# Optimization experiments

Hardware: AMD Instinct MI355X
Metric: run time of the kernel (lower is better)

## Reference

```python
import jax, jax.numpy as jnp
import numpy as np

P = 100   # num_proxies
N = 1024  # num_samples
D = 512


def _edge_index():
    # complete bipartite proxy<->sample graph, both directions, plus self-loops
    # (PyG GATConv adds self-loops for all nodes by default)
    p = np.arange(P)
    s = np.arange(P, P + N)
    src_ps = np.repeat(p, N)   # proxy -> sample
    dst_ps = np.tile(s, P)
    loops = np.arange(P + N)
    src = np.concatenate([src_ps, dst_ps, loops]).astype(np.int32)
    dst = np.concatenate([dst_ps, src_ps, loops]).astype(np.int32)
    return jnp.asarray(src), jnp.asarray(dst)


def setup_inputs() -> dict:
    key = jax.random.key(0)
    ks = jax.random.split(key, 10)
    sc = 1.0 / np.sqrt(D)
    src, dst = _edge_index()
    return {
        "x": jax.random.normal(ks[0], (N, D), jnp.float32),
        "proxies": jax.random.normal(ks[1], (P, D), jnp.float32),
        "W1": jax.random.normal(ks[2], (D, D), jnp.float32) * sc,
        "a_src1": jax.random.normal(ks[3], (D,), jnp.float32) * sc,
        "a_dst1": jax.random.normal(ks[4], (D,), jnp.float32) * sc,
        "b1": jnp.zeros((D,), jnp.float32),
        "W2": jax.random.normal(ks[5], (D, D), jnp.float32) * sc,
        "a_src2": jax.random.normal(ks[6], (D,), jnp.float32) * sc,
        "a_dst2": jax.random.normal(ks[7], (D,), jnp.float32) * sc,
        "b2": jnp.zeros((D,), jnp.float32),
        "fc_w": jax.random.normal(ks[8], (D, 100), jnp.float32) * sc,
        "fc_b": jnp.zeros((100,), jnp.float32),
        "src": src,
        "dst": dst,
    }


def _gat_conv(x, src, dst, W, a_src, a_dst, b, n_nodes):
    # PyG GATConv, heads=1, concat=True, negative_slope=0.2
    h = x @ W                      # [n, D]
    l_src = h @ a_src              # [n]
    l_dst = h @ a_dst              # [n]
    e = jax.nn.leaky_relu(l_src[src] + l_dst[dst], 0.2)   # [E]
    # segment softmax over edges sharing the same destination
    e = e - jax.ops.segment_max(e, dst, num_segments=n_nodes)[dst]
    ex = jnp.exp(e)
    denom = jax.ops.segment_sum(ex, dst, num_segments=n_nodes)[dst]
    alpha = ex / denom             # [E]
    out = jax.ops.segment_sum(alpha[:, None] * h[src], dst, num_segments=n_nodes)
    return out + b


def reference(x, proxies, W1, a_src1, a_dst1, b1, W2, a_src2, a_dst2, b2, fc_w, fc_b, src, dst):
    n = P + N
    h = jnp.concatenate([proxies, x], axis=0)          # [P+N, D]
    h = jax.nn.relu(_gat_conv(h, src, dst, W1, a_src1, a_dst1, b1, n))
    # Dropout -> identity (eval)
    h = jax.nn.relu(_gat_conv(h, src, dst, W2, a_src2, a_dst2, b2, n))
    preds = h @ fc_w + fc_b                            # [P+N, 100]
    return preds[P:], h[P:]
```

## Files before the change

kernel.cpp:

```cpp
#include <hip/hip_runtime.h>

#define PP 100
#define NS 1024
#define NN 1124
#define DD 512
#define CC 100
#define NTHR 256

typedef _Float16 f16;
typedef _Float16 f16x8 __attribute__((ext_vector_type(8)));
typedef float    f32x4 __attribute__((ext_vector_type(4)));

__device__ __forceinline__ float lk(float v) { return v > 0.f ? v : 0.2f * v; }
__device__ __forceinline__ f16 hif(float v) { return (f16)v; }
__device__ __forceinline__ f16 lof(float v) { return (f16)(v - (float)((f16)v)); }


__device__ __forceinline__ void mgemm_core(
    const f16* __restrict__ Ah, const f16* __restrict__ Al,
    const f16* __restrict__ Bth, const f16* __restrict__ Btl,
    int K, int row0, int col0, f16* __restrict__ lds, f32x4 acc[2][2])
{
  const int t = threadIdx.x;
  const int lane = t & 63, w = t >> 6;
  const int wr = w >> 1, wc = w & 1;
  const int srow = t >> 2, su = t & 3;
  const size_t aoff = (size_t)(row0 + srow) * K + su * 8;
  const size_t boff = (size_t)(col0 + srow) * K + su * 8;
  const int lw = srow * 40 + su * 8;
  const int fra = wr * 32 + (lane & 15);
  const int frb = wc * 32 + (lane & 15);
  const int fu  = (lane >> 4) * 8;
  f32x4 pa0 = *(const f32x4*)(Ah + aoff);
  f32x4 pa1 = *(const f32x4*)(Al + aoff);
  f32x4 pb0 = *(const f32x4*)(Bth + boff);
  f32x4 pb1 = *(const f32x4*)(Btl + boff);
  *(f32x4*)(lds + 0    + lw) = pa0;
  *(f32x4*)(lds + 2560 + lw) = pa1;
  *(f32x4*)(lds + 5120 + lw) = pb0;
  *(f32x4*)(lds + 7680 + lw) = pb1;
  if (K > 32) {
    pa0 = *(const f32x4*)(Ah + aoff + 32);
    pa1 = *(const f32x4*)(Al + aoff + 32);
    pb0 = *(const f32x4*)(Bth + boff + 32);
    pb1 = *(const f32x4*)(Btl + boff + 32);
  }
  __syncthreads();
  int cur = 0;
  for (int kt = 32; kt <= K; kt += 32) {
    f16* rb = lds + cur * 10240;
    f16* wb = lds + (cur ^ 1) * 10240;
    f16x8 ah[2], al[2], bh[2], bl[2];
#pragma unroll
    for (int m = 0; m < 2; ++m) {
      ah[m] = *(const f16x8*)(rb + (fra + m * 16) * 40 + fu);
      al[m] = *(const f16x8*)(rb + 2560 + (fra + m * 16) * 40 + fu);
    }
#pragma unroll
    for (int n = 0; n < 2; ++n) {
      bh[n] = *(const f16x8*)(rb + 5120 + (frb + n * 16) * 40 + fu);
      bl[n] = *(const f16x8*)(rb + 7680 + (frb + n * 16) * 40 + fu);
    }
    if (kt < K) {
      *(f32x4*)(wb + 0    + lw) = pa0;
      *(f32x4*)(wb + 2560 + lw) = pa1;
      *(f32x4*)(wb + 5120 + lw) = pb0;
      *(f32x4*)(wb + 7680 + lw) = pb1;
      if (kt + 32 < K) {
        pa0 = *(const f32x4*)(Ah + aoff + kt + 32);
        pa1 = *(const f32x4*)(Al + aoff + kt + 32);
        pb0 = *(const f32x4*)(Bth + boff + kt + 32);
        pb1 = *(const f32x4*)(Btl + boff + kt + 32);
      }
    }
#pragma unroll
    for (int m = 0; m < 2; ++m)
#pragma unroll
      for (int n = 0; n < 2; ++n) {
        acc[m][n] = __builtin_amdgcn_mfma_f32_16x16x32_f16(ah[m], bh[n], acc[m][n], 0, 0, 0);
        acc[m][n] = __builtin_amdgcn_mfma_f32_16x16x32_f16(al[m], bh[n], acc[m][n], 0, 0, 0);
        acc[m][n] = __builtin_amdgcn_mfma_f32_16x16x32_f16(ah[m], bl[n], acc[m][n], 0, 0, 0);
      }
    __syncthreads();
    cur ^= 1;
  }
}

__device__ __forceinline__ void agg_core(
    const float* __restrict__ lsrc, int kvalid,
    const float* __restrict__ ldb, const float* __restrict__ lsb,
    const f16* __restrict__ Bth, const f16* __restrict__ Btl,
    int K, int row0, int col0, int rvalid,
    const float* __restrict__ selfv,
    f16* __restrict__ outh, f16* __restrict__ outl,
    f16* __restrict__ lds, float* __restrict__ fred)
{
  const int t = threadIdx.x, lane = t & 63, w = t >> 6;
  const int wr = w >> 1, wc = w & 1;
  float* zred = fred;
  float* res  = fred + 256;
  float* riz  = fred + 320;
  const int srow = t >> 2, su = t & 3;
  float sm = -1e30f;
  for (int k = t; k < kvalid; k += NTHR) sm = fmaxf(sm, lsrc[k]);
#pragma unroll
  for (int off = 1; off < 64; off <<= 1) sm = fmaxf(sm, __shfl_xor(sm, off));
  if (lane == 0) zred[w] = sm;
  __syncthreads();
  sm = fmaxf(fmaxf(zred[0], zred[1]), fmaxf(zred[2], zred[3]));
  __syncthreads();
  const bool rok = (row0 + srow) < rvalid;
  float ldr = 0.f, mr = 0.f;
  if (rok) {
    ldr = ldb[row0 + srow];
    mr  = lk(fmaxf(sm, lsb[row0 + srow]) + ldr);
  }
  const size_t boff = (size_t)(col0 + srow) * K + su * 8;
  const int lw = srow * 40 + su * 8;
  const int fra = wr * 32 + (lane & 15);
  const int frb = wc * 32 + (lane & 15);
  const int fu  = (lane >> 4) * 8;
  f32x4 acc[2][2] = {};
  float zacc = 0.f;
  f32x4 pl0 = *(const f32x4*)(lsrc + su * 8);
  f32x4 pl1 = *(const f32x4*)(lsrc + su * 8 + 4);
  f32x4 pb0 = *(const f32x4*)(Bth + boff);
  f32x4 pb1 = *(const f32x4*)(Btl + boff);
  {
    f16x8 ae, al8;
#pragma unroll
    for (int j = 0; j < 8; ++j) {
      const int k = su * 8 + j;
      const float lv = (j < 4) ? pl0[j] : pl1[j - 4];
      float f = 0.f;
      if (rok && k < kvalid) f = __expf(lk(lv + ldr) - mr);
      zacc += f;
      ae[j] = hif(f); al8[j] = lof(f);
    }
    *(f16x8*)(lds + 0    + lw) = ae;
    *(f16x8*)(lds + 2560 + lw) = al8;
    *(f32x4*)(lds + 5120 + lw) = pb0;
    *(f32x4*)(lds + 7680 + lw) = pb1;
  }
  if (K > 32) {
    pl0 = *(const f32x4*)(lsrc + 32 + su * 8);
    pl1 = *(const f32x4*)(lsrc + 32 + su * 8 + 4);
    pb0 = *(const f32x4*)(Bth + boff + 32);
    pb1 = *(const f32x4*)(Btl + boff + 32);
  }
  __syncthreads();
  int cur = 0;
  for (int kt = 32; kt <= K; kt += 32) {
    f16* rb = lds + cur * 10240;
    f16* wb = lds + (cur ^ 1) * 10240;
    f16x8 ah[2], alr[2], bh[2], bl[2];
#pragma unroll
    for (int m = 0; m < 2; ++m) {
      ah[m]  = *(const f16x8*)(rb + (fra + m * 16) * 40 + fu);
      alr[m] = *(const f16x8*)(rb + 2560 + (fra + m * 16) * 40 + fu);
    }
#pragma unroll
    for (int n = 0; n < 2; ++n) {
      bh[n] = *(const f16x8*)(rb + 5120 + (frb + n * 16) * 40 + fu);
      bl[n] = *(const f16x8*)(rb + 7680 + (frb + n * 16) * 40 + fu);
    }
    if (kt < K) {
      f16x8 ae, al8;
      const int k0 = kt + su * 8;
#pragma unroll
      for (int j = 0; j < 8; ++j) {
        const int k = k0 + j;
        const float lv = (j < 4) ? pl0[j] : pl1[j - 4];
        float f = 0.f;
        if (rok && k < kvalid) f = __expf(lk(lv + ldr) - mr);
        zacc += f;
        ae[j] = hif(f); al8[j] = lof(f);
      }
      *(f16x8*)(wb + 0    + lw) = ae;
      *(f16x8*)(wb + 2560 + lw) = al8;
      *(f32x4*)(wb + 5120 + lw) = pb0;
      *(f32x4*)(wb + 7680 + lw) = pb1;
      if (kt + 32 < K) {
        pl0 = *(const f32x4*)(lsrc + kt + 32 + su * 8);
        pl1 = *(const f32x4*)(lsrc + kt + 32 + su * 8 + 4);
        pb0 = *(const f32x4*)(Bth + boff + kt + 32);
        pb1 = *(const f32x4*)(Btl + boff + kt + 32);
      }
    }
#pragma unroll
    for (int m = 0; m < 2; ++m)
#pragma unroll
      for (int n = 0; n < 2; ++n) {
        acc[m][n] = __builtin_amdgcn_mfma_f32_16x16x32_f16(ah[m],  bh[n], acc[m][n], 0, 0, 0);
        acc[m][n] = __builtin_amdgcn_mfma_f32_16x16x32_f16(alr[m], bh[n], acc[m][n], 0, 0, 0);
        acc[m][n] = __builtin_amdgcn_mfma_f32_16x16x32_f16(ah[m],  bl[n], acc[m][n], 0, 0, 0);
      }
    __syncthreads();
    cur ^= 1;
  }
  zred[t] = zacc;
  __syncthreads();
  if (t < 64) {
    float z = zred[t * 4] + zred[t * 4 + 1] + zred[t * 4 + 2] + zred[t * 4 + 3];
    float es = 0.f, iz = 0.f;
    if (row0 + t < rvalid) {
      const float l2 = ldb[row0 + t], s2 = lsb[row0 + t];
      const float m2 = lk(fmaxf(sm, s2) + l2);
      es = __expf(lk(s2 + l2) - m2);
      iz = 1.f / (z + es);
    }
    res[t] = es; riz[t] = iz;
  }
  __syncthreads();
#pragma unroll
  for (int m = 0; m < 2; ++m)
#pragma unroll
    for (int q = 0; q < 4; ++q) {
      const int rl = wr * 32 + m * 16 + (lane >> 4) * 4 + q;
      const int gr = row0 + rl;
      if (gr >= rvalid) continue;
      const float es = res[rl], iz = riz[rl];
#pragma unroll
      for (int n = 0; n < 2; ++n) {
        const int c = col0 + wc * 32 + n * 16 + (lane & 15);
        const float v = (acc[m][n][q] + es * selfv[(size_t)gr * DD + c]) * iz;
        outh[(size_t)gr * DD + c] = hif(v);
        outl[(size_t)gr * DD + c] = lof(v);
      }
    }
}

__device__ __forceinline__ void cvt_tile(
    const float* __restrict__ in, int R, int Cin,
    f16* __restrict__ oh, f16* __restrict__ ol, int ldo,
    int ti, int tj)
{
  const int t = threadIdx.x;
  const int gj0 = tj * 64 + (t & 31) * 2;
  const int i8  = (t >> 5) * 8;
  const bool c0 = gj0 < Cin, c1 = (gj0 + 1) < Cin;
  f16x8 vh0, vl0, vh1, vl1;
#pragma unroll
  for (int e = 0; e < 8; ++e) {
    const int gi = ti * 64 + i8 + e;
    float a = 0.f, b = 0.f;
    if (gi < R) {
      if (c0 && c1) {
        const float2 v = *(const float2*)(in + (size_t)gi * Cin + gj0);
        a = v.x; b = v.y;
      } else if (c0) {
        a = in[(size_t)gi * Cin + gj0];
      }
    }
    vh0[e] = hif(a); vl0[e] = lof(a);
    vh1[e] = hif(b); vl1[e] = lof(b);
  }
  const size_t o0 = (size_t)gj0 * ldo + ti * 64 + i8;
  *(f16x8*)(oh + o0) = vh0;
  *(f16x8*)(ol + o0) = vl0;
  const size_t o1 = o0 + ldo;
  *(f16x8*)(oh + o1) = vh1;
  *(f16x8*)(ol + o1) = vl1;
}

__global__ __launch_bounds__(NTHR) void prep1_k(
    const float* __restrict__ W1, const float* __restrict__ W2,
    const float* __restrict__ as1, const float* __restrict__ ad1,
    const float* __restrict__ as2, const float* __restrict__ ad2,
    float* __restrict__ v1s, float* __restrict__ v1d,
    float* __restrict__ v2s, float* __restrict__ v2d,
    float* __restrict__ ls2, float* __restrict__ ld2)
{
  const int u = blockIdx.x;
  if (u < 256) {
    const int wid  = u * 4 + (threadIdx.x >> 6);
    const int lane = threadIdx.x & 63;
    const int r = wid & 511;
    const bool l1 = (wid < 512);
    const float* W = l1 ? W1 : W2;
    const float4* a4 = (const float4*)(l1 ? as1 : as2);
    const float4* b4 = (const float4*)(l1 ? ad1 : ad2);
    const float4* w4 = (const float4*)(W + (size_t)r * DD);
    float4 w0 = w4[lane], w1 = w4[lane + 64];
    float4 a0 = a4[lane], a1 = a4[lane + 64];
    float4 b0 = b4[lane], b1 = b4[lane + 64];
    float s1 = w0.x * a0.x + w0.y * a0.y + w0.z * a0.z + w0.w * a0.w
             + w1.x * a1.x + w1.y * a1.y + w1.z * a1.z + w1.w * a1.w;
    float s2 = w0.x * b0.x + w0.y * b0.y + w0.z * b0.z + w0.w * b0.w
             + w1.x * b1.x + w1.y * b1.y + w1.z * b1.z + w1.w * b1.w;
#pragma unroll
    for (int off = 32; off > 0; off >>= 1) {
      s1 += __shfl_down(s1, off);
      s2 += __shfl_down(s2, off);
    }
    if (lane == 0) {
      (l1 ? v1s : v2s)[r] = s1;
      (l1 ? v1d : v2d)[r] = s2;
    }
  } else {
    for (int i = threadIdx.x; i < 1152; i += NTHR) { ls2[i] = 0.f; ld2[i] = 0.f; }
  }
}

__global__ __launch_bounds__(NTHR) void prep2_k(
    const float* __restrict__ x, const float* __restrict__ prox,
    const float* __restrict__ W1, const float* __restrict__ W2,
    const float* __restrict__ fcw,
    const float* __restrict__ v1s, const float* __restrict__ v1d,
    f16* xth, f16* xtl, f16* pth, f16* ptl,
    f16* W1th, f16* W1tl, f16* W2th, f16* W2tl, f16* fwth, f16* fwtl,
    float* __restrict__ ls1, float* __restrict__ ld1)
{
  const int b = blockIdx.x;
  if (b < 64) {
    cvt_tile(W1, 512, 512, W1th, W1tl, 512, b >> 3, b & 7);
  } else if (b < 128) {
    cvt_tile(W2, 512, 512, W2th, W2tl, 512, (b - 64) >> 3, (b - 64) & 7);
  } else if (b < 256) {
    cvt_tile(x, NS, 512, xth, xtl, NS, (b - 128) >> 3, (b - 128) & 7);
  } else if (b < 272) {
    cvt_tile(prox, PP, 512, pth, ptl, 128, (b - 256) >> 3, (b - 256) & 7);
  } else if (b < 288) {
    cvt_tile(fcw, 512, CC, fwth, fwtl, 512, (b - 272) >> 1, (b - 272) & 1);
  } else {
    const int r    = (b - 288) * 4 + (threadIdx.x >> 6);
    const int lane = threadIdx.x & 63;
    if (r >= NN) return;
    const float* row = (r < PP) ? prox + (size_t)r * DD
                                : x + (size_t)(r - PP) * DD;
    const float4* r4 = (const float4*)row;
    const float4* s4 = (const float4*)v1s;
    const float4* d4 = (const float4*)v1d;
    float4 v0 = r4[lane], v1 = r4[lane + 64];
    float4 a0 = s4[lane], a1 = s4[lane + 64];
    float4 b0 = d4[lane], b1 = d4[lane + 64];
    float s1 = v0.x * a0.x + v0.y * a0.y + v0.z * a0.z + v0.w * a0.w
             + v1.x * a1.x + v1.y * a1.y + v1.z * a1.z + v1.w * a1.w;
    float s2 = v0.x * b0.x + v0.y * b0.y + v0.z * b0.z + v0.w * b0.w
             + v1.x * b1.x + v1.y * b1.y + v1.z * b1.z + v1.w * b1.w;
#pragma unroll
    for (int off = 32; off > 0; off >>= 1) {
      s1 += __shfl_down(s1, off);
      s2 += __shfl_down(s2, off);
    }
    if (lane == 0) { ls1[r] = s1; ld1[r] = s2; }
  }
}

__global__ __launch_bounds__(NTHR) void agg1x_k(
    const float* __restrict__ ls1, const float* __restrict__ ld1,
    const f16* __restrict__ pth, const f16* __restrict__ ptl,
    const f16* __restrict__ xth, const f16* __restrict__ xtl,
    const float* __restrict__ x, const float* __restrict__ prox,
    f16* __restrict__ M1h, f16* __restrict__ M1l)
{
  __shared__ __align__(16) f16 lds[20480];
  __shared__ float fred[384];
  const int b = blockIdx.x;
  if (b < 128) {
    const int row0 = (b >> 3) * 64, col0 = (b & 7) * 64;
    agg_core(ls1, PP, ld1 + PP, ls1 + PP, pth, ptl, 128, row0, col0, NS,
             x, M1h + (size_t)PP * DD, M1l + (size_t)PP * DD, lds, fred);
  } else {
    const int b2 = b - 128;
    const int row0 = (b2 >> 3) * 64, col0 = (b2 & 7) * 64;
    agg_core(ls1 + PP, NS, ld1, ls1, xth, xtl, NS, row0, col0, PP,
             prox, M1h, M1l, lds, fred);
  }
}

__global__ __launch_bounds__(NTHR) void h1_k(
    const f16* __restrict__ M1h, const f16* __restrict__ M1l,
    const f16* __restrict__ W1th, const f16* __restrict__ W1tl,
    const float* __restrict__ b1,
    const float* __restrict__ v2s, const float* __restrict__ v2d,
    float* __restrict__ h1, f16* __restrict__ h1pth, f16* __restrict__ h1ptl,
    float* __restrict__ ls2, float* __restrict__ ld2)
{
  __shared__ __align__(16) f16 lds[20480];
  f32x4 acc[2][2] = {};
  const int t = threadIdx.x, lane = t & 63, w = t >> 6, wr = w >> 1, wc = w & 1;
  const int b = blockIdx.x;
  const int row0 = (b >> 3) * 64, col0 = (b & 7) * 64;
  mgemm_core(M1h, M1l, W1th, W1tl, DD, row0, col0, lds, acc);
  const int c0 = col0 + wc * 32 + (lane & 15);
  const int c1 = c0 + 16;
  const float vs0 = v2s[c0], vs1 = v2s[c1];
  const float vd0 = v2d[c0], vd1 = v2d[c1];
  const float bb0 = b1[c0],  bb1 = b1[c1];
#pragma unroll
  for (int m = 0; m < 2; ++m)
#pragma unroll
    for (int q = 0; q < 4; ++q) {
      const int r = row0 + wr * 32 + m * 16 + (lane >> 4) * 4 + q;
      if (r >= NN) continue;
      float ps = 0.f, pd = 0.f;
#pragma unroll
      for (int n = 0; n < 2; ++n) {
        const int c = (n == 0) ? c0 : c1;
        const float v = fmaxf(acc[m][n][q] + (n == 0 ? bb0 : bb1), 0.f);
        h1[(size_t)r * DD + c] = v;
        ps += v * (n == 0 ? vs0 : vs1);
        pd += v * (n == 0 ? vd0 : vd1);
        if (r < 128) {
          const size_t o = (size_t)c * 128 + r;
          f16 hh = (f16)0.f, ll = (f16)0.f;
          if (r < PP) { hh = hif(v); ll = lof(v); }
          h1pth[o] = hh; h1ptl[o] = ll;
        }
      }
#pragma unroll
      for (int off = 1; off < 16; off <<= 1) {
        ps += __shfl_xor(ps, off);
        pd += __shfl_xor(pd, off);
      }
      if ((lane & 15) == 0) {
        atomicAdd(&ls2[r], ps);
        atomicAdd(&ld2[r], pd);
      }
    }
}

__global__ __launch_bounds__(NTHR) void agg2x_k(
    const float* __restrict__ ls2, const float* __restrict__ ld2,
    const f16* __restrict__ h1pth, const f16* __restrict__ h1ptl,
    const float* __restrict__ h1,
    f16* __restrict__ M2h, f16* __restrict__ M2l)
{
  __shared__ __align__(16) f16 lds[20480];
  __shared__ float fred[384];
  const int b = blockIdx.x;
  const int row0 = (b >> 3) * 64, col0 = (b & 7) * 64;
  agg_core(ls2, PP, ld2 + PP, ls2 + PP, h1pth, h1ptl, 128, row0, col0, NS,
           h1 + (size_t)PP * DD, M2h, M2l, lds, fred);
}

__global__ __launch_bounds__(NTHR) void h2_k(
    const f16* __restrict__ M2h, const f16* __restrict__ M2l,
    const f16* __restrict__ W2th, const f16* __restrict__ W2tl,
    const float* __restrict__ b2, float* __restrict__ h2s,
    f16* __restrict__ h2h, f16* __restrict__ h2l)
{
  __shared__ __align__(16) f16 lds[20480];
  f32x4 acc[2][2] = {};
  const int t = threadIdx.x, lane = t & 63, w = t >> 6, wr = w >> 1, wc = w & 1;
  const int b = blockIdx.x;
  const int row0 = (b >> 3) * 64, col0 = (b & 7) * 64;
  mgemm_core(M2h, M2l, W2th, W2tl, DD, row0, col0, lds, acc);
#pragma unroll
  for (int m = 0; m < 2; ++m)
#pragma unroll
    for (int q = 0; q < 4; ++q) {
      const int r = row0 + wr * 32 + m * 16 + (lane >> 4) * 4 + q;
#pragma unroll
      for (int n = 0; n < 2; ++n) {
        const int c = col0 + wc * 32 + n * 16 + (lane & 15);
        const float v = fmaxf(acc[m][n][q] + b2[c], 0.f);
        const size_t o = (size_t)r * DD + c;
        h2s[o] = v;
        h2h[o] = hif(v); h2l[o] = lof(v);
      }
    }
}

__global__ __launch_bounds__(NTHR) void fc_k(
    const f16* __restrict__ h2h, const f16* __restrict__ h2l,
    const f16* __restrict__ fwth, const f16* __restrict__ fwtl,
    const float* __restrict__ fcb, float* __restrict__ out)
{
  __shared__ __align__(16) f16 lds[20480];
  f32x4 acc[2][2] = {};
  const int t = threadIdx.x, lane = t & 63, w = t >> 6, wr = w >> 1, wc = w & 1;
  const int b = blockIdx.x;
  const int row0 = (b >> 1) * 64, col0 = (b & 1) * 64;
  mgemm_core(h2h, h2l, fwth, fwtl, DD, row0, col0, lds, acc);
#pragma unroll
  for (int m = 0; m < 2; ++m)
#pragma unroll
    for (int q = 0; q < 4; ++q) {
      const int r = row0 + wr * 32 + m * 16 + (lane >> 4) * 4 + q;
#pragma unroll
      for (int n = 0; n < 2; ++n) {
        const int c = col0 + wc * 32 + n * 16 + (lane & 15);
        if (c < CC) out[(size_t)r * CC + c] = acc[m][n][q] + fcb[c];
      }
    }
}

extern "C" void kernel_launch(void* const* d_in, const int* in_sizes, int n_in,
                              void* d_out, int out_size, void* d_ws, size_t ws_size,
                              hipStream_t stream)
{
  const float* x    = (const float*)d_in[0];
  const float* prox = (const float*)d_in[1];
  const float* W1   = (const float*)d_in[2];
  const float* as1  = (const float*)d_in[3];
  const float* ad1  = (const float*)d_in[4];
  const float* b1   = (const float*)d_in[5];
  const float* W2   = (const float*)d_in[6];
  const float* as2  = (const float*)d_in[7];
  const float* ad2  = (const float*)d_in[8];
  const float* b2   = (const float*)d_in[9];
  const float* fcw  = (const float*)d_in[10];
  const float* fcb  = (const float*)d_in[11];
  float* out = (float*)d_out;

  float* F = (float*)d_ws;
  float* h1   = F; F += (size_t)NN * DD;
  float* ls1  = F; F += 1152;
  float* ld1  = F; F += 1152;
  float* ls2  = F; F += 1152;
  float* ld2  = F; F += 1152;
  float* v1s  = F; F += DD;
  float* v1d  = F; F += DD;
  float* v2s  = F; F += DD;
  float* v2d  = F; F += DD;
  f16* H = (f16*)F;
  f16* M1h  = H; H += (size_t)1152 * DD;
  f16* M1l  = H; H += (size_t)1152 * DD;
  f16* M2h  = H; H += (size_t)NS * DD;
  f16* M2l  = H; H += (size_t)NS * DD;
  f16* xth  = H; H += (size_t)DD * NS;
  f16* xtl  = H; H += (size_t)DD * NS;
  f16* pth  = H; H += (size_t)DD * 128;
  f16* ptl  = H; H += (size_t)DD * 128;
  f16* W1th = H; H += (size_t)DD * DD;
  f16* W1tl = H; H += (size_t)DD * DD;
  f16* W2th = H; H += (size_t)DD * DD;
  f16* W2tl = H; H += (size_t)DD * DD;
  f16* fwth = H; H += (size_t)128 * DD;
  f16* fwtl = H; H += (size_t)128 * DD;
  f16* h2h  = H; H += (size_t)NS * DD;
  f16* h2l  = H; H += (size_t)NS * DD;
  f16* h1pth = H; H += (size_t)DD * 128;
  f16* h1ptl = H; H += (size_t)DD * 128;
  float* h2s = out + (size_t)NS * CC;

  dim3 blk(NTHR);
  prep1_k<<<dim3(257), blk, 0, stream>>>(W1, W2, as1, ad1, as2, ad2,
                                         v1s, v1d, v2s, v2d, ls2, ld2);
  prep2_k<<<dim3(569), blk, 0, stream>>>(x, prox, W1, W2, fcw, v1s, v1d,
      xth, xtl, pth, ptl, W1th, W1tl, W2th, W2tl, fwth, fwtl, ls1, ld1);
  agg1x_k<<<dim3(144), blk, 0, stream>>>(ls1, ld1, pth, ptl, xth, xtl,
                                         x, prox, M1h, M1l);
  h1_k<<<dim3(144), blk, 0, stream>>>(M1h, M1l, W1th, W1tl, b1, v2s, v2d,
                                      h1, h1pth, h1ptl, ls2, ld2);
  agg2x_k<<<dim3(128), blk, 0, stream>>>(ls2, ld2, h1pth, h1ptl, h1, M2h, M2l);
  h2_k<<<dim3(128), blk, 0, stream>>>(M2h, M2l, W2th, W2tl, b2, h2s, h2h, h2l);
  fc_k<<<dim3(32), blk, 0, stream>>>(h2h, h2l, fwth, fwtl, fcb, out);
}
```

Measured before the change: 151.6 us.

## Split proxy-row aggregation over K chunks with atomics, normalize in h1 GEMM

The proxy-destination aggregation in layer 1 (100 rows summing over 1024 samples) used to be done by 16 blocks each running the full K=1024 loop. It now splits K into four 256-wide chunks across 64 blocks. Each block atomically adds its unnormalized partial sums into an fp32 buffer, along with the softmax denominators. The self-loop term and the 1/Z normalization move into the h1 GEMM's A-tile load, which converts the fp32 partials to split f16 on the fly. The cost is extra zeroing blocks in prep1, fp32 atomics, and more per-tile work in h1_k.

```diff
diff --git a/kernel.cpp b/kernel.cpp
--- a/kernel.cpp
+++ b/kernel.cpp
@@ -269,7 +269,8 @@
     const float* __restrict__ as2, const float* __restrict__ ad2,
     float* __restrict__ v1s, float* __restrict__ v1d,
     float* __restrict__ v2s, float* __restrict__ v2d,
-    float* __restrict__ ls2, float* __restrict__ ld2)
+    float* __restrict__ ls2, float* __restrict__ ld2,
+    float* __restrict__ M1pf, float* __restrict__ zP)
 {
   const int u = blockIdx.x;
   if (u < 256) {
@@ -297,8 +298,16 @@
       (l1 ? v1s : v2s)[r] = s1;
       (l1 ? v1d : v2d)[r] = s2;
     }
+  } else if (u == 256) {
+    for (int i = threadIdx.x; i < 1152; i += NTHR) { ls2[i] = 0.f; ld2[i] = 0.f; }
+    if (threadIdx.x < 128) zP[threadIdx.x] = 0.f;
   } else {
-    for (int i = threadIdx.x; i < 1152; i += NTHR) { ls2[i] = 0.f; ld2[i] = 0.f; }
+    float4* p4 = (float4*)M1pf + (size_t)(u - 257) * 800;
+#pragma unroll
+    for (int p = 0; p < 4; ++p) {
+      const int i = threadIdx.x + p * 256;
+      if (i < 800) p4[i] = make_float4(0.f, 0.f, 0.f, 0.f);
+    }
   }
 }
 
@@ -351,7 +360,8 @@
     const float* __restrict__ ls1, const float* __restrict__ ld1,
     const f16* __restrict__ pth, const f16* __restrict__ ptl,
     const f16* __restrict__ xth, const f16* __restrict__ xtl,
-    const float* __restrict__ x, const float* __restrict__ prox,
+    const float* __restrict__ x,
+    float* __restrict__ M1pf, float* __restrict__ zP,
     f16* __restrict__ M1h, f16* __restrict__ M1l)
 {
   __shared__ __align__(16) f16 lds[20480];
@@ -361,16 +371,138 @@
     const int row0 = (b >> 3) * 64, col0 = (b & 7) * 64;
     agg_core(ls1, PP, ld1 + PP, ls1 + PP, pth, ptl, 128, row0, col0, NS,
              x, M1h + (size_t)PP * DD, M1l + (size_t)PP * DD, lds, fred);
-  } else {
-    const int b2 = b - 128;
-    const int row0 = (b2 >> 3) * 64, col0 = (b2 & 7) * 64;
-    agg_core(ls1 + PP, NS, ld1, ls1, xth, xtl, NS, row0, col0, PP,
-             prox, M1h, M1l, lds, fred);
-  }
+    return;
+  }
+  const int t = threadIdx.x, lane = t & 63, w = t >> 6;
+  const int wr = w >> 1, wc = w & 1;
+  const int b2 = b - 128;
+  const int tile = b2 >> 2, chunk = b2 & 3;
+  const int row0 = (tile >> 3) * 64, col0 = (tile & 7) * 64;
+  const int k0 = chunk * 256;
+  const float* lsrc = ls1 + PP;
+  float sm = -1e30f;
+  for (int k = t; k < NS; k += NTHR) sm = fmaxf(sm, lsrc[k]);
+#pragma unroll
+  for (int off = 1; off < 64; off <<= 1) sm = fmaxf(sm, __shfl_xor(sm, off));
+  if (lane == 0) fred[w] = sm;
+  __syncthreads();
+  sm = fmaxf(fmaxf(fred[0], fred[1]), fmaxf(fred[2], fred[3]));
+  __syncthreads();
+  const int srow = t >> 2, su = t & 3;
+  const bool rok = (row0 + srow) < PP;
+  float ldr = 0.f, mr = 0.f;
+  if (rok) {
+    ldr = ld1[row0 + srow];
+    mr  = lk(fmaxf(sm, ls1[row0 + srow]) + ldr);
+  }
+  const size_t boff = (size_t)(col0 + srow) * NS + k0 + su * 8;
+  const int lw = srow * 40 + su * 8;
+  const int fra = wr * 32 + (lane & 15);
+  const int frb = wc * 32 + (lane & 15);
+  const int fu  = (lane >> 4) * 8;
+  f32x4 acc[2][2] = {};
+  float zacc = 0.f;
+  f32x4 pl0 = *(const f32x4*)(lsrc + k0 + su * 8);
+  f32x4 pl1 = *(const f32x4*)(lsrc + k0 + su * 8 + 4);
+  f32x4 pb0 = *(const f32x4*)(xth + boff);
+  f32x4 pb1 = *(const f32x4*)(xtl + boff);
+  {
+    f16x8 ae, al8;
+#pragma unroll
+    for (int j = 0; j < 8; ++j) {
+      const float lv = (j < 4) ? pl0[j] : pl1[j - 4];
+      float f = 0.f;
+      if (rok) f = __expf(lk(lv + ldr) - mr);
+      zacc += f;
+      ae[j] = hif(f); al8[j] = lof(f);
+    }
+    *(f16x8*)(lds + 0    + lw) = ae;
+    *(f16x8*)(lds + 2560 + lw) = al8;
+    *(f32x4*)(lds + 5120 + lw) = pb0;
+    *(f32x4*)(lds + 7680 + lw) = pb1;
+  }
+  pl0 = *(const f32x4*)(lsrc + k0 + 32 + su * 8);
+  pl1 = *(const f32x4*)(lsrc + k0 + 32 + su * 8 + 4);
+  pb0 = *(const f32x4*)(xth + boff + 32);
+  pb1 = *(const f32x4*)(xtl + boff + 32);
+  __syncthreads();
+  int cur = 0;
+  for (int kt = 32; kt <= 256; kt += 32) {
+    f16* rb = lds + cur * 10240;
+    f16* wb = lds + (cur ^ 1) * 10240;
+    f16x8 ah[2], alr[2], bh[2], bl[2];
+#pragma unroll
+    for (int m = 0; m < 2; ++m) {
+      ah[m]  = *(const f16x8*)(rb + (fra + m * 16) * 40 + fu);
+      alr[m] = *(const f16x8*)(rb + 2560 + (fra + m * 16) * 40 + fu);
+    }
+#pragma unroll
+    for (int n = 0; n < 2; ++n) {
+      bh[n] = *(const f16x8*)(rb + 5120 + (frb + n * 16) * 40 + fu);
+      bl[n] = *(const f16x8*)(rb + 7680 + (frb + n * 16) * 40 + fu);
+    }
+    if (kt < 256) {
+      f16x8 ae, al8;
+#pragma unroll
+      for (int j = 0; j < 8; ++j) {
+        const float lv = (j < 4) ? pl0[j] : pl1[j - 4];
+        float f = 0.f;
+        if (rok) f = __expf(lk(lv + ldr) - mr);
+        zacc += f;
+        ae[j] = hif(f); al8[j] = lof(f);
+      }
+      *(f16x8*)(wb + 0    + lw) = ae;
+      *(f16x8*)(wb + 2560 + lw) = al8;
+      *(f32x4*)(wb + 5120 + lw) = pb0;
+      *(f32x4*)(wb + 7680 + lw) = pb1;
+      if (kt + 32 < 256) {
+        pl0 = *(const f32x4*)(lsrc + k0 + kt + 32 + su * 8);
+        pl1 = *(const f32x4*)(lsrc + k0 + kt + 32 + su * 8 + 4);
+        pb0 = *(const f32x4*)(xth + boff + kt + 32);
+        pb1 = *(const f32x4*)(xtl + boff + kt + 32);
+      }
+    }
+#pragma unroll
+    for (int m = 0; m < 2; ++m)
+#pragma unroll
+      for (int n = 0; n < 2; ++n) {
+        acc[m][n] = __builtin_amdgcn_mfma_f32_16x16x32_f16(ah[m],  bh[n], acc[m][n], 0, 0, 0);
+        acc[m][n] = __builtin_amdgcn_mfma_f32_16x16x32_f16(alr[m], bh[n], acc[m][n], 0, 0, 0);
+        acc[m][n] = __builtin_amdgcn_mfma_f32_16x16x32_f16(ah[m],  bl[n], acc[m][n], 0, 0, 0);
+      }
+    __syncthreads();
+    cur ^= 1;
+  }
+  if (col0 == 0) {
+    fred[t] = zacc;
+    __syncthreads();
+    if (t < 64) {
+      const int r = row0 + t;
+      if (r < PP) {
+        float z = fred[t * 4] + fred[t * 4 + 1] + fred[t * 4 + 2] + fred[t * 4 + 3];
+        atomicAdd(&zP[r], z);
+      }
+    }
+  }
+#pragma unroll
+  for (int m = 0; m < 2; ++m)
+#pragma unroll
+    for (int q = 0; q < 4; ++q) {
+      const int gr = row0 + wr * 32 + m * 16 + (lane >> 4) * 4 + q;
+      if (gr >= PP) continue;
+#pragma unroll
+      for (int n = 0; n < 2; ++n) {
+        const int c = col0 + wc * 32 + n * 16 + (lane & 15);
+        atomicAdd(&M1pf[(size_t)gr * DD + c], acc[m][n][q]);
+      }
+    }
 }
 
 __global__ __launch_bounds__(NTHR) void h1_k(
     const f16* __restrict__ M1h, const f16* __restrict__ M1l,
+    const float* __restrict__ M1pf, const float* __restrict__ zP,
+    const float* __restrict__ ls1, const float* __restrict__ ld1,
+    const float* __restrict__ prox,
     const f16* __restrict__ W1th, const f16* __restrict__ W1tl,
     const float* __restrict__ b1,
     const float* __restrict__ v2s, const float* __restrict__ v2d,
@@ -378,11 +510,121 @@
     float* __restrict__ ls2, float* __restrict__ ld2)
 {
   __shared__ __align__(16) f16 lds[20480];
-  f32x4 acc[2][2] = {};
+  __shared__ float fred[384];
+  float* esA = fred + 256;
+  float* izA = fred + 320;
   const int t = threadIdx.x, lane = t & 63, w = t >> 6, wr = w >> 1, wc = w & 1;
   const int b = blockIdx.x;
   const int row0 = (b >> 3) * 64, col0 = (b & 7) * 64;
-  mgemm_core(M1h, M1l, W1th, W1tl, DD, row0, col0, lds, acc);
+  const bool hasP = (row0 < 128);
+  if (hasP) {
+    float sm = -1e30f;
+    for (int k = t; k < NS; k += NTHR) sm = fmaxf(sm, ls1[PP + k]);
+#pragma unroll
+    for (int off = 1; off < 64; off <<= 1) sm = fmaxf(sm, __shfl_xor(sm, off));
+    if (lane == 0) fred[w] = sm;
+    __syncthreads();
+    sm = fmaxf(fmaxf(fred[0], fred[1]), fmaxf(fred[2], fred[3]));
+    if (t < 64) {
+      const int r = row0 + t;
+      float es = 0.f, iz = 0.f;
+      if (r < PP) {
+        const float ldr = ld1[r];
+        const float m = lk(fmaxf(sm, ls1[r]) + ldr);
+        es = __expf(lk(ls1[r] + ldr) - m);
+        iz = 1.f / (zP[r] + es);
+      }
+      esA[t] = es; izA[t] = iz;
+    }
+    __syncthreads();
+  }
+  const int srow = t >> 2, su = t & 3;
+  const int ar = row0 + srow;
+  const bool isP = ar < PP;
+  const size_t aoff = (size_t)ar * DD + su * 8;
+  const size_t boff = (size_t)(col0 + srow) * DD + su * 8;
+  const int lw = srow * 40 + su * 8;
+  const int fra = wr * 32 + (lane & 15);
+  const int frb = wc * 32 + (lane & 15);
+  const int fu  = (lane >> 4) * 8;
+  const float esr = isP ? esA[srow] : 0.f;
+  const float izr = isP ? izA[srow] : 0.f;
+  f32x4 qa0, qa1, qb0, qb1, pb0, pb1;
+  auto loadA = [&](int k) {
+    if (isP) {
+      qa0 = *(const f32x4*)(M1pf + aoff + k);
+      qa1 = *(const f32x4*)(M1pf + aoff + k + 4);
+      qb0 = *(const f32x4*)(prox + aoff + k);
+      qb1 = *(const f32x4*)(prox + aoff + k + 4);
+    } else {
+      qa0 = *(const f32x4*)(M1h + aoff + k);
+      qa1 = *(const f32x4*)(M1l + aoff + k);
+    }
+  };
+  auto storeA = [&](f16* wb) {
+    if (isP) {
+      f16x8 hh, ll;
+#pragma unroll
+      for (int j = 0; j < 8; ++j) {
+        const float pv = (j < 4) ? qa0[j] : qa1[j - 4];
+        const float xv = (j < 4) ? qb0[j] : qb1[j - 4];
+        const float v = (pv + esr * xv) * izr;
+        hh[j] = hif(v); ll[j] = lof(v);
+      }
+      *(f16x8*)(wb + lw) = hh;
+      *(f16x8*)(wb + 2560 + lw) = ll;
+    } else {
+      *(f32x4*)(wb + lw) = qa0;
+      *(f32x4*)(wb + 2560 + lw) = qa1;
+    }
+  };
+  f32x4 acc[2][2] = {};
+  loadA(0);
+  pb0 = *(const f32x4*)(W1th + boff);
+  pb1 = *(const f32x4*)(W1tl + boff);
+  storeA(lds);
+  *(f32x4*)(lds + 5120 + lw) = pb0;
+  *(f32x4*)(lds + 7680 + lw) = pb1;
+  loadA(32);
+  pb0 = *(const f32x4*)(W1th + boff + 32);
+  pb1 = *(const f32x4*)(W1tl + boff + 32);
+  __syncthreads();
+  int cur = 0;
+  for (int kt = 32; kt <= DD; kt += 32) {
+    f16* rb = lds + cur * 10240;
+    f16* wb = lds + (cur ^ 1) * 10240;
+    f16x8 ah[2], al[2], bh[2], bl[2];
+#pragma unroll
+    for (int m = 0; m < 2; ++m) {
+      ah[m] = *(const f16x8*)(rb + (fra + m * 16) * 40 + fu);
+      al[m] = *(const f16x8*)(rb + 2560 + (fra + m * 16) * 40 + fu);
+    }
+#pragma unroll
+    for (int n = 0; n < 2; ++n) {
+      bh[n] = *(const f16x8*)(rb + 5120 + (frb + n * 16) * 40 + fu);
+      bl[n] = *(const f16x8*)(rb + 7680 + (frb + n * 16) * 40 + fu);
+    }
+    if (kt < DD) {
+      storeA(wb);
+      *(f32x4*)(wb + 5120 + lw) = pb0;
+      *(f32x4*)(wb + 7680 + lw) = pb1;
+      if (kt + 32 < DD) {
+        loadA(kt + 32);
+        pb0 = *(const f32x4*)(W1th + boff + kt + 32);
+        pb1 = *(const f32x4*)(W1tl + boff + kt + 32);
+      }
+    }
+#pragma unroll
+    for (int m = 0; m < 2; ++m)
+#pragma unroll
+      for (int n = 0; n < 2; ++n) {
+        acc[m][n] = __builtin_amdgcn_mfma_f32_16x16x32_f16(ah[m], bh[n], acc[m][n], 0, 0, 0);
+        acc[m][n] = __builtin_amdgcn_mfma_f32_16x16x32_f16(al[m], bh[n], acc[m][n], 0, 0, 0);
+        acc[m][n] = __builtin_amdgcn_mfma_f32_16x16x32_f16(ah[m], bl[n], acc[m][n], 0, 0, 0);
+      }
+    __syncthreads();
+    cur ^= 1;
+  }
   const int c0 = col0 + wc * 32 + (lane & 15);
   const int c1 = c0 + 16;
   const float vs0 = v2s[c0], vs1 = v2s[c1];
@@ -515,6 +757,8 @@
   float* v1d  = F; F += DD;
   float* v2s  = F; F += DD;
   float* v2d  = F; F += DD;
+  float* M1pf = F; F += (size_t)128 * DD;
+  float* zP   = F; F += 128;
   f16* H = (f16*)F;
   f16* M1h  = H; H += (size_t)1152 * DD;
   f16* M1l  = H; H += (size_t)1152 * DD;
@@ -537,13 +781,15 @@
   float* h2s = out + (size_t)NS * CC;
 
   dim3 blk(NTHR);
-  prep1_k<<<dim3(257), blk, 0, stream>>>(W1, W2, as1, ad1, as2, ad2,
-                                         v1s, v1d, v2s, v2d, ls2, ld2);
+  prep1_k<<<dim3(273), blk, 0, stream>>>(W1, W2, as1, ad1, as2, ad2,
+                                         v1s, v1d, v2s, v2d, ls2, ld2,
+                                         M1pf, zP);
   prep2_k<<<dim3(569), blk, 0, stream>>>(x, prox, W1, W2, fcw, v1s, v1d,
       xth, xtl, pth, ptl, W1th, W1tl, W2th, W2tl, fwth, fwtl, ls1, ld1);
-  agg1x_k<<<dim3(144), blk, 0, stream>>>(ls1, ld1, pth, ptl, xth, xtl,
-                                         x, prox, M1h, M1l);
-  h1_k<<<dim3(144), blk, 0, stream>>>(M1h, M1l, W1th, W1tl, b1, v2s, v2d,
+  agg1x_k<<<dim3(192), blk, 0, stream>>>(ls1, ld1, pth, ptl, xth, xtl,
+                                         x, M1pf, zP, M1h, M1l);
+  h1_k<<<dim3(144), blk, 0, stream>>>(M1h, M1l, M1pf, zP, ls1, ld1, prox,
+                                      W1th, W1tl, b1, v2s, v2d,
                                       h1, h1pth, h1ptl, ls2, ld2);
   agg2x_k<<<dim3(128), blk, 0, stream>>>(ls2, ld2, h1pth, h1ptl, h1, M2h, M2l);
   h2_k<<<dim3(128), blk, 0, stream>>>(M2h, M2l, W2th, W2tl, b2, h2s, h2h, h2l);
```

Measured after the change: 141.9 us. -6.4%, faster.
